# Performance work log

Measured on AMD Instinct MI355X. Metric: run time of the kernel, lower is better.

The kernel has to match this reference:

```python
import jax, jax.numpy as jnp
import numpy as np

KERNEL_MUL = 2.0
KERNEL_NUM = 5
EPS = 1e-8


def _l2_normalize(x):
    # F.normalize(p=2, dim=-1): x / max(||x||, 1e-12)
    norm = jnp.sqrt(jnp.sum(x * x, axis=-1, keepdims=True))
    return x / jnp.maximum(norm, 1e-12)


def _mmd(source, target):
    n_s = source.shape[0]
    n_t = target.shape[0]
    s = _l2_normalize(source)
    t = _l2_normalize(target)
    total = jnp.concatenate([s, t], axis=0)  # [n, d]
    n = n_s + n_t
    # pairwise squared L2 via norm-expansion trick (avoids [n,n,d] intermediate)
    sq = jnp.sum(total * total, axis=-1)  # [n]
    gram = total @ total.T                # [n, n]
    d2 = jnp.maximum(sq[:, None] + sq[None, :] - 2.0 * gram, 0.0)
    # bandwidth from detached distances (torch uses .data)
    d2_ng = jax.lax.stop_gradient(d2)
    bandwidth = jnp.sum(d2_ng) / (n * n - n) + EPS
    bandwidth = bandwidth / (KERNEL_MUL ** (KERNEL_NUM // 2))
    kernels = jnp.zeros_like(d2)
    for i in range(KERNEL_NUM):
        kernels = kernels + jnp.exp(-d2 / (bandwidth * KERNEL_MUL ** i))
    XX = kernels[:n_s, :n_s]
    YY = kernels[n_s:, n_s:]
    XY = kernels[:n_s, n_s:]
    loss = (jnp.sum(XX) - jnp.trace(XX)) / (n_s * (n_s - 1))
    loss = loss + (jnp.sum(YY) - jnp.trace(YY)) / (n_t * (n_t - 1))
    loss = loss - 2.0 * jnp.sum(XY) / (n_s * n_t)
    return loss


def setup_inputs() -> dict:
    key = jax.random.key(0)
    k1, k2 = jax.random.split(key)
    source = jax.random.normal(k1, (4096, 512), dtype=jnp.float32)
    target = jax.random.normal(k2, (4096, 512), dtype=jnp.float32)
    return {"source": source, "target": target}


def reference(source, target):
    return _mmd(source, target)
```

## Files before the change

kernel.cpp:

```cpp
#include <hip/hip_runtime.h>

#define D 512
#define NS 4096
#define NROWS 8192
#define NB_XX 272
#define NB_GEMM (2 * NB_XX + 512)
#define LDSS 24576

typedef __attribute__((ext_vector_type(8))) short bf16x8;
typedef __attribute__((ext_vector_type(4))) float f32x4;

__device__ __forceinline__ unsigned short f2bf(float f) {
  unsigned int u = __float_as_uint(f);
  u += 0x7fffu + ((u >> 16) & 1u);
  return (unsigned short)(u >> 16);
}
__device__ __forceinline__ float bf2f(unsigned short h) {
  return __uint_as_float(((unsigned int)h) << 16);
}
__device__ __forceinline__ void gload_lds16(const void* g, void* l) {
  __builtin_amdgcn_global_load_lds(
      (const __attribute__((address_space(1))) unsigned int*)g,
      (__attribute__((address_space(3))) unsigned int*)l, 16, 0, 0);
}
#define WAITV(N) asm volatile("s_waitcnt vmcnt(" #N ")" ::: "memory")

__global__ __launch_bounds__(512) void k_pre(const float* __restrict__ src,
                                             const float* __restrict__ tgt,
                                             float* __restrict__ sq,
                                             unsigned short* __restrict__ hi,
                                             unsigned short* __restrict__ lo,
                                             float* __restrict__ Spart) {
  int t = threadIdx.x, w = t >> 6, l = t & 63;
  float csum[8] = {0.f, 0.f, 0.f, 0.f, 0.f, 0.f, 0.f, 0.f};
  for (int i = 0; i < 16; ++i) {
    int r = blockIdx.x * 128 + w * 16 + i;
    const float* p = (r < NS) ? (src + (size_t)r * D) : (tgt + (size_t)(r - NS) * D);
    float4 v0 = *(const float4*)(p + l * 8);
    float4 v1 = *(const float4*)(p + l * 8 + 4);
    float x[8] = {v0.x, v0.y, v0.z, v0.w, v1.x, v1.y, v1.z, v1.w};
    float s = 0.f;
    #pragma unroll
    for (int j = 0; j < 8; ++j) s += x[j] * x[j];
    #pragma unroll
    for (int off = 1; off < 64; off <<= 1) s += __shfl_xor(s, off);
    float iv = 1.0f / fmaxf(sqrtf(s), 1e-12f);
    if (l == 0) sq[r] = s * iv * iv;
    unsigned short hs[8], ls[8];
    #pragma unroll
    for (int j = 0; j < 8; ++j) {
      float xn = x[j] * iv;
      unsigned short h = f2bf(xn);
      hs[j] = h;
      ls[j] = f2bf(xn - bf2f(h));
      csum[j] += xn;
    }
    *(uint4*)&hi[(size_t)r * D + l * 8] = *(uint4*)hs;
    *(uint4*)&lo[(size_t)r * D + l * 8] = *(uint4*)ls;
  }
  __shared__ float cs[8][512];
  #pragma unroll
  for (int j = 0; j < 8; ++j) cs[w][l * 8 + j] = csum[j];
  __syncthreads();
  float a = 0.f;
  #pragma unroll
  for (int ww = 0; ww < 8; ++ww) a += cs[ww][t];
  Spart[blockIdx.x * 512 + t] = a;
}

__global__ __launch_bounds__(512) void k_prep(const float* __restrict__ sq,
                                              const float* __restrict__ Spart,
                                              float* __restrict__ na,
                                              double* __restrict__ dsum,
                                              unsigned int* __restrict__ cnt) {
  int t = threadIdx.x;
  double ssq = 0.0;
  for (int i = t; i < NROWS; i += 512) ssq += (double)sq[i];
  double cssum = 0.0;
  for (int b = 0; b < 64; ++b) cssum += (double)Spart[b * 512 + t];
  double ss2 = cssum * cssum;
  #pragma unroll
  for (int off = 32; off; off >>= 1) {
    ssq += __shfl_down(ssq, off);
    ss2 += __shfl_down(ss2, off);
  }
  __shared__ double l1[8], l2[8];
  if ((t & 63) == 0) { l1[t >> 6] = ssq; l2[t >> 6] = ss2; }
  __syncthreads();
  if (t == 0) {
    double SSQ = 0.0, SS2 = 0.0;
    #pragma unroll
    for (int i = 0; i < 8; ++i) { SSQ += l1[i]; SS2 += l2[i]; }
    double n = (double)NROWS;
    double sum_d2 = 2.0 * n * SSQ - 2.0 * SS2;
    double bw = sum_d2 / (n * n - n) + 1e-8;
    bw = bw * 0.25;
    const double LOG2E = 1.4426950408889634;
    #pragma unroll
    for (int m = 0; m < 5; ++m) na[m] = (float)(-LOG2E / (bw * (double)(1 << m)));
    dsum[0] = 0.0; dsum[1] = 0.0; dsum[2] = 0.0;
    cnt[0] = 0u;
  }
}

__global__ __launch_bounds__(512, 2) void k_gemm(const unsigned short* __restrict__ hi,
                                                 const unsigned short* __restrict__ lo,
                                                 const float* __restrict__ sq,
                                                 const float* __restrict__ na,
                                                 double* __restrict__ dsum,
                                                 unsigned int* __restrict__ cnt,
                                                 float* __restrict__ out) {
  __shared__ unsigned short lds[3 * LDSS];
  __shared__ double red[8];

  int bid0 = blockIdx.x;
  int bid = (bid0 & 7) * (NB_GEMM / 8) + (bid0 >> 3);
  int type, bi, c2;
  if (bid < 2 * NB_XX) {
    type = (bid >= NB_XX);
    int idx = bid - type * NB_XX;
    int b = 0;
    while (idx >= 16 - (b >> 1)) { idx -= 16 - (b >> 1); ++b; }
    bi = b;
    c2 = (b >> 1) + idx;
  } else {
    type = 2;
    int rem = bid - 2 * NB_XX;
    bi = rem >> 4;
    c2 = rem & 15;
  }
  int offA = (type == 1) ? NS : 0;
  int offB = (type == 0) ? 0 : NS;
  bool sym = (type < 2);

  int t = threadIdx.x;
  int w = t >> 6, l = t & 63;
  int wr = w >> 2, wc = w & 3;
  int fr = l & 15, fk = l >> 4;

  const unsigned short* gsrc[6];
  int ldsoff[6];
  #pragma unroll
  for (int c = 0; c < 6; ++c) {
    int r = w * 6 + c;
    int isB = (r >= 16);
    int isLo = isB ? (r >= 32) : (r >= 8);
    int rr = isB ? ((r - 16) & 15) : (r & 7);
    int rowbase = isB ? (offB + c2 * 256 + rr * 16) : (offA + bi * 128 + rr * 16);
    const unsigned short* arr = isLo ? lo : hi;
    int gswz = ((l & 3) ^ ((l >> 3) & 3)) * 8;
    gsrc[c] = arr + (size_t)(rowbase + (l >> 2)) * D + gswz;
    ldsoff[c] = r * 512;
  }

  int rsw = (fr >> 1) & 3;
  int aoff = (wr * 64 + fr) * 32 + (fk ^ rsw) * 8;
  int boff = 8192 + (wc * 64 + fr) * 32 + (fk ^ rsw) * 8;

  f32x4 acc[4][4];
  f32x4 zero = {0.f, 0.f, 0.f, 0.f};
  #pragma unroll
  for (int m = 0; m < 4; ++m)
    #pragma unroll
    for (int n = 0; n < 4; ++n) acc[m][n] = zero;

  #pragma unroll
  for (int c = 0; c < 6; ++c) gload_lds16(gsrc[c], &lds[ldsoff[c]]);
  #pragma unroll
  for (int c = 0; c < 6; ++c) gload_lds16(gsrc[c] + 32, &lds[LDSS + ldsoff[c]]);

  unsigned int b0 = 0, b1 = LDSS, b2 = 2 * LDSS;
  for (int kt = 0; kt < 16; ++kt) {
    if (kt < 15) { WAITV(6); } else { WAITV(0); }
    __builtin_amdgcn_s_barrier();
    __builtin_amdgcn_sched_barrier(0);

    bf16x8 ah[4], al[4], bh[4], bl[4];
    #pragma unroll
    for (int m = 0; m < 4; ++m) {
      ah[m] = *(const bf16x8*)&lds[b0 + aoff + m * 512];
      al[m] = *(const bf16x8*)&lds[b0 + 4096 + aoff + m * 512];
    }
    #pragma unroll
    for (int n = 0; n < 4; ++n) {
      bh[n] = *(const bf16x8*)&lds[b0 + boff + n * 512];
      bl[n] = *(const bf16x8*)&lds[b0 + 8192 + boff + n * 512];
    }
    if (kt < 14) {
      #pragma unroll
      for (int c = 0; c < 6; ++c)
        gload_lds16(gsrc[c] + (kt + 2) * 32, &lds[b2 + ldsoff[c]]);
    }
    __builtin_amdgcn_s_setprio(1);
    #pragma unroll
    for (int m = 0; m < 4; ++m)
      #pragma unroll
      for (int n = 0; n < 4; ++n) {
        acc[m][n] = __builtin_amdgcn_mfma_f32_16x16x32_bf16(ah[m], bh[n], acc[m][n], 0, 0, 0);
        acc[m][n] = __builtin_amdgcn_mfma_f32_16x16x32_bf16(ah[m], bl[n], acc[m][n], 0, 0, 0);
        acc[m][n] = __builtin_amdgcn_mfma_f32_16x16x32_bf16(al[m], bh[n], acc[m][n], 0, 0, 0);
      }
    __builtin_amdgcn_s_setprio(0);
    unsigned int tmp = b0; b0 = b1; b1 = b2; b2 = tmp;
  }

  float nam[5];
  #pragma unroll
  for (int m2 = 0; m2 < 5; ++m2) nam[m2] = na[m2];
  int giL0 = bi * 128 + wr * 64;
  int gjL0 = c2 * 256 + wc * 64;
  float sqa[4][4], sqb[4];
  #pragma unroll
  for (int m = 0; m < 4; ++m)
    #pragma unroll
    for (int j = 0; j < 4; ++j) sqa[m][j] = sq[offA + giL0 + m * 16 + fk * 4 + j];
  #pragma unroll
  for (int n = 0; n < 4; ++n) sqb[n] = sq[offB + gjL0 + n * 16 + fr];

  double local = 0.0;
  #pragma unroll
  for (int m = 0; m < 4; ++m)
    #pragma unroll
    for (int n = 0; n < 4; ++n) {
      int gjL = gjL0 + n * 16 + fr;
      #pragma unroll
      for (int j = 0; j < 4; ++j) {
        int giL = giL0 + m * 16 + fk * 4 + j;
        float d2 = fmaxf(fmaf(-2.f, acc[m][n][j], sqa[m][j] + sqb[n]), 0.f);
        float kv = 0.f;
        #pragma unroll
        for (int m2 = 0; m2 < 5; ++m2) kv += __builtin_amdgcn_exp2f(d2 * nam[m2]);
        float wf = sym ? ((gjL > giL) ? 2.f : ((gjL == giL) ? 1.f : 0.f)) : 1.f;
        local += (double)(wf * kv);
      }
    }
  #pragma unroll
  for (int off = 32; off; off >>= 1) local += __shfl_down(local, off);
  if (l == 0) red[w] = local;
  __syncthreads();
  if (t == 0) {
    double bsum = 0.0;
    #pragma unroll
    for (int i = 0; i < 8; ++i) bsum += red[i];
    atomicAdd(&dsum[type], bsum);
    __threadfence();
    unsigned int ticket = atomicAdd(cnt, 1u);
    if (ticket == NB_GEMM - 1) {
      __threadfence();
      double A0 = dsum[0], A1 = dsum[1], A2 = dsum[2];
      double ns = (double)NS;
      double loss = (A0 - 5.0 * ns) / (ns * (ns - 1.0))
                  + (A1 - 5.0 * ns) / (ns * (ns - 1.0))
                  - 2.0 * A2 / (ns * ns);
      out[0] = (float)loss;
    }
  }
}

extern "C" void kernel_launch(void* const* d_in, const int* in_sizes, int n_in,
                              void* d_out, int out_size, void* d_ws, size_t ws_size,
                              hipStream_t stream) {
  (void)in_sizes; (void)n_in; (void)out_size; (void)ws_size;
  const float* src = (const float*)d_in[0];
  const float* tgt = (const float*)d_in[1];
  float* out = (float*)d_out;
  char* ws = (char*)d_ws;

  float*          sq    = (float*)(ws);
  float*          Spart = (float*)(ws + 0x8000);
  float*          na    = (float*)(ws + 0x28000);
  double*         dsum  = (double*)(ws + 0x28040);
  unsigned int*   cnt   = (unsigned int*)(ws + 0x28080);
  unsigned short* hi    = (unsigned short*)(ws + 0x100000);
  unsigned short* lo    = (unsigned short*)(ws + 0x900000);

  hipLaunchKernelGGL(k_pre, dim3(64), dim3(512), 0, stream, src, tgt, sq, hi, lo, Spart);
  hipLaunchKernelGGL(k_prep, dim3(1), dim3(512), 0, stream, sq, Spart, na, dsum, cnt);
  hipLaunchKernelGGL(k_gemm, dim3(NB_GEMM), dim3(512), 0, stream, hi, lo, sq, na, dsum, cnt, out);
}
```

Measured before the change: 232.4 us.

## Switch split-bf16 gram to int8 hi/lo fixed-point MFMA with persistent tile queue

Normalized rows are quantized to 14-bit fixed point and split into int8 high and low halves. The gram matrix is then computed with i8 MFMA (16x16x64) into exact int32 accumulators and recombined in double, replacing the three-pass bf16 hi/lo scheme. The GEMM also becomes a persistent kernel of 256 blocks that pull tiles from an atomic queue, with prefetch of the next tile's data overlapping the current tile's tail. Squared norms are recomputed from the quantized integers so the distances stay consistent. The trade-off is four MFMAs per step instead of three, at higher int8 throughput and half the bytes, plus quantization error and more register pressure from three accumulator sets.

Result: slower. 354.6 us (+52.5%).

```diff
diff --git a/kernel.cpp b/kernel.cpp
--- a/kernel.cpp
+++ b/kernel.cpp
@@ -4,20 +4,13 @@
 #define NS 4096
 #define NROWS 8192
 #define NB_XX 272
-#define NB_GEMM (2 * NB_XX + 512)
-#define LDSS 24576
-
-typedef __attribute__((ext_vector_type(8))) short bf16x8;
-typedef __attribute__((ext_vector_type(4))) float f32x4;
-
-__device__ __forceinline__ unsigned short f2bf(float f) {
-  unsigned int u = __float_as_uint(f);
-  u += 0x7fffu + ((u >> 16) & 1u);
-  return (unsigned short)(u >> 16);
-}
-__device__ __forceinline__ float bf2f(unsigned short h) {
-  return __uint_as_float(((unsigned int)h) << 16);
-}
+#define NB (2 * NB_XX + 512)
+#define NPB 256
+#define LDSB 49152
+#define LA_OFF 0x400000u
+
+typedef __attribute__((ext_vector_type(4))) int i32x4;
+
 __device__ __forceinline__ void gload_lds16(const void* g, void* l) {
   __builtin_amdgcn_global_load_lds(
       (const __attribute__((address_space(1))) unsigned int*)g,
@@ -28,8 +21,8 @@
 __global__ __launch_bounds__(512) void k_pre(const float* __restrict__ src,
                                              const float* __restrict__ tgt,
                                              float* __restrict__ sq,
-                                             unsigned short* __restrict__ hi,
-                                             unsigned short* __restrict__ lo,
+                                             signed char* __restrict__ ha,
+                                             signed char* __restrict__ la,
                                              float* __restrict__ Spart) {
   int t = threadIdx.x, w = t >> 6, l = t & 63;
   float csum[8] = {0.f, 0.f, 0.f, 0.f, 0.f, 0.f, 0.f, 0.f};
@@ -45,18 +38,24 @@
     #pragma unroll
     for (int off = 1; off < 64; off <<= 1) s += __shfl_xor(s, off);
     float iv = 1.0f / fmaxf(sqrtf(s), 1e-12f);
-    if (l == 0) sq[r] = s * iv * iv;
-    unsigned short hs[8], ls[8];
+    signed char hs[8], ls[8];
+    int sxx = 0;
     #pragma unroll
     for (int j = 0; j < 8; ++j) {
       float xn = x[j] * iv;
-      unsigned short h = f2bf(xn);
-      hs[j] = h;
-      ls[j] = f2bf(xn - bf2f(h));
+      int X = __float2int_rn(xn * 16384.f);
+      int h = (X + 128) >> 8;
+      int lo = X - (h << 8);
+      hs[j] = (signed char)h;
+      ls[j] = (signed char)lo;
+      sxx += X * X;
       csum[j] += xn;
     }
-    *(uint4*)&hi[(size_t)r * D + l * 8] = *(uint4*)hs;
-    *(uint4*)&lo[(size_t)r * D + l * 8] = *(uint4*)ls;
+    #pragma unroll
+    for (int off = 1; off < 64; off <<= 1) sxx += __shfl_xor(sxx, off);
+    if (l == 0) sq[r] = (float)((double)sxx * (1.0 / 268435456.0));
+    *(uint2*)&ha[(size_t)r * 512 + l * 8] = *(uint2*)hs;
+    *(uint2*)&la[(size_t)r * 512 + l * 8] = *(uint2*)ls;
   }
   __shared__ float cs[8][512];
   #pragma unroll
@@ -72,7 +71,8 @@
                                               const float* __restrict__ Spart,
                                               float* __restrict__ na,
                                               double* __restrict__ dsum,
-                                              unsigned int* __restrict__ cnt) {
+                                              unsigned int* __restrict__ qcnt,
+                                              unsigned int* __restrict__ ccnt) {
   int t = threadIdx.x;
   double ssq = 0.0;
   for (int i = t; i < NROWS; i += 512) ssq += (double)sq[i];
@@ -99,153 +99,231 @@
     #pragma unroll
     for (int m = 0; m < 5; ++m) na[m] = (float)(-LOG2E / (bw * (double)(1 << m)));
     dsum[0] = 0.0; dsum[1] = 0.0; dsum[2] = 0.0;
-    cnt[0] = 0u;
-  }
-}
-
-__global__ __launch_bounds__(512, 2) void k_gemm(const unsigned short* __restrict__ hi,
-                                                 const unsigned short* __restrict__ lo,
-                                                 const float* __restrict__ sq,
-                                                 const float* __restrict__ na,
-                                                 double* __restrict__ dsum,
-                                                 unsigned int* __restrict__ cnt,
-                                                 float* __restrict__ out) {
-  __shared__ unsigned short lds[3 * LDSS];
-  __shared__ double red[8];
-
-  int bid0 = blockIdx.x;
-  int bid = (bid0 & 7) * (NB_GEMM / 8) + (bid0 >> 3);
-  int type, bi, c2;
+    qcnt[0] = 0u; ccnt[0] = 0u;
+  }
+}
+
+__device__ __forceinline__ void decode_tile(int bid, int& type, int& bi, int& c2,
+                                            int& offA, int& offB, int& sym) {
   if (bid < 2 * NB_XX) {
     type = (bid >= NB_XX);
     int idx = bid - type * NB_XX;
     int b = 0;
     while (idx >= 16 - (b >> 1)) { idx -= 16 - (b >> 1); ++b; }
-    bi = b;
-    c2 = (b >> 1) + idx;
+    bi = b; c2 = (b >> 1) + idx; sym = 1;
   } else {
     type = 2;
     int rem = bid - 2 * NB_XX;
-    bi = rem >> 4;
-    c2 = rem & 15;
-  }
-  int offA = (type == 1) ? NS : 0;
-  int offB = (type == 0) ? 0 : NS;
-  bool sym = (type < 2);
+    bi = rem >> 4; c2 = rem & 15; sym = 0;
+  }
+  offA = (type == 1) ? NS : 0;
+  offB = (type == 0) ? 0 : NS;
+}
+
+__global__ __launch_bounds__(512, 2) void k_gemm(const signed char* __restrict__ ha,
+                                                 const float* __restrict__ sq,
+                                                 const float* __restrict__ na,
+                                                 double* __restrict__ dsum,
+                                                 unsigned int* __restrict__ qcnt,
+                                                 unsigned int* __restrict__ ccnt,
+                                                 float* __restrict__ out) {
+  __shared__ signed char lds[3 * LDSB];
+  __shared__ int tslot[2];
+  __shared__ double red[8];
 
   int t = threadIdx.x;
   int w = t >> 6, l = t & 63;
   int wr = w >> 2, wc = w & 3;
   int fr = l & 15, fk = l >> 4;
-
-  const unsigned short* gsrc[6];
-  int ldsoff[6];
+  int rsw = (fr >> 1) & 3;
+
+  unsigned offc[6];
+  int isb[6];
+  int gsw = ((l & 3) ^ ((l >> 3) & 3)) * 16;
   #pragma unroll
   for (int c = 0; c < 6; ++c) {
     int r = w * 6 + c;
     int isB = (r >= 16);
     int isLo = isB ? (r >= 32) : (r >= 8);
-    int rr = isB ? ((r - 16) & 15) : (r & 7);
-    int rowbase = isB ? (offB + c2 * 256 + rr * 16) : (offA + bi * 128 + rr * 16);
-    const unsigned short* arr = isLo ? lo : hi;
-    int gswz = ((l & 3) ^ ((l >> 3) & 3)) * 8;
-    gsrc[c] = arr + (size_t)(rowbase + (l >> 2)) * D + gswz;
-    ldsoff[c] = r * 512;
-  }
-
-  int rsw = (fr >> 1) & 3;
-  int aoff = (wr * 64 + fr) * 32 + (fk ^ rsw) * 8;
-  int boff = 8192 + (wc * 64 + fr) * 32 + (fk ^ rsw) * 8;
-
-  f32x4 acc[4][4];
-  f32x4 zero = {0.f, 0.f, 0.f, 0.f};
+    int rr16 = isB ? ((r - 16) & 15) : (r & 7);
+    offc[c] = (isLo ? LA_OFF : 0u) + (unsigned)((rr16 * 16 + (l >> 2)) * 512 + gsw);
+    isb[c] = isB;
+  }
+  int ldsw = w * 6 * 1024;
+  int aRd = (wr * 4) * 1024 + fr * 64 + ((fk ^ rsw) * 16);
+  int bRd = 16384 + (wc * 4) * 1024 + fr * 64 + ((fk ^ rsw) * 16);
+
+  float nam0 = na[0], nam1 = na[1], nam2 = na[2], nam3 = na[3], nam4 = na[4];
+
+  i32x4 acc1[4][4], acc2[4][4], acc3[4][4];
+  i32x4 izero = {0, 0, 0, 0};
   #pragma unroll
   for (int m = 0; m < 4; ++m)
     #pragma unroll
-    for (int n = 0; n < 4; ++n) acc[m][n] = zero;
-
-  #pragma unroll
-  for (int c = 0; c < 6; ++c) gload_lds16(gsrc[c], &lds[ldsoff[c]]);
-  #pragma unroll
-  for (int c = 0; c < 6; ++c) gload_lds16(gsrc[c] + 32, &lds[LDSS + ldsoff[c]]);
-
-  unsigned int b0 = 0, b1 = LDSS, b2 = 2 * LDSS;
-  for (int kt = 0; kt < 16; ++kt) {
-    if (kt < 15) { WAITV(6); } else { WAITV(0); }
-    __builtin_amdgcn_s_barrier();
-    __builtin_amdgcn_sched_barrier(0);
-
-    bf16x8 ah[4], al[4], bh[4], bl[4];
-    #pragma unroll
-    for (int m = 0; m < 4; ++m) {
-      ah[m] = *(const bf16x8*)&lds[b0 + aoff + m * 512];
-      al[m] = *(const bf16x8*)&lds[b0 + 4096 + aoff + m * 512];
-    }
-    #pragma unroll
-    for (int n = 0; n < 4; ++n) {
-      bh[n] = *(const bf16x8*)&lds[b0 + boff + n * 512];
-      bl[n] = *(const bf16x8*)&lds[b0 + 8192 + boff + n * 512];
-    }
-    if (kt < 14) {
-      #pragma unroll
-      for (int c = 0; c < 6; ++c)
-        gload_lds16(gsrc[c] + (kt + 2) * 32, &lds[b2 + ldsoff[c]]);
-    }
-    __builtin_amdgcn_s_setprio(1);
-    #pragma unroll
-    for (int m = 0; m < 4; ++m)
+    for (int n = 0; n < 4; ++n) { acc1[m][n] = izero; acc2[m][n] = izero; acc3[m][n] = izero; }
+
+  double dl0 = 0.0, dl1 = 0.0, dl2 = 0.0;
+
+  if (t == 0) {
+    tslot[0] = (int)atomicAdd(qcnt, 1u);
+    tslot[1] = (int)atomicAdd(qcnt, 1u);
+  }
+  __syncthreads();
+  int cur = __builtin_amdgcn_readfirstlane(tslot[0]);
+  int nxt = __builtin_amdgcn_readfirstlane(tslot[1]);
+
+  int typeC = 0, biC = 0, c2C = 0, oAC = 0, oBC = 0, symC = 0;
+  unsigned tbA_c = 0, tbB_c = 0, tbA_n = 0, tbB_n = 0;
+  if (cur < NB) {
+    decode_tile(cur, typeC, biC, c2C, oAC, oBC, symC);
+    tbA_c = (unsigned)(oAC + biC * 128) * 512u;
+    tbB_c = (unsigned)(oBC + c2C * 256) * 512u;
+  }
+  if (nxt < NB) {
+    int t2, b2, cc2, a2, o2, s2;
+    decode_tile(nxt, t2, b2, cc2, a2, o2, s2);
+    tbA_n = (unsigned)(a2 + b2 * 128) * 512u;
+    tbB_n = (unsigned)(o2 + cc2 * 256) * 512u;
+  }
+
+  if (cur < NB) {
+    #pragma unroll
+    for (int c = 0; c < 6; ++c)
+      gload_lds16(ha + (size_t)(offc[c] + (isb[c] ? tbB_c : tbA_c)), &lds[0 + ldsw + c * 1024]);
+    #pragma unroll
+    for (int c = 0; c < 6; ++c)
+      gload_lds16(ha + (size_t)(offc[c] + (isb[c] ? tbB_c : tbA_c) + 64u), &lds[LDSB + ldsw + c * 1024]);
+  }
+
+  unsigned sb0 = 0, sb1 = LDSB, sb2 = 2 * LDSB;
+  int pend = NB;
+
+  while (cur < NB) {
+    bool nxtv = (nxt < NB);
+    for (int kt = 0; kt < 8; ++kt) {
+      if (kt == 7 && !nxtv) { WAITV(0); } else { WAITV(6); }
+      __builtin_amdgcn_s_barrier();
+      __builtin_amdgcn_sched_barrier(0);
+      if (kt == 0) {
+        if (t == 0) {
+          int v = (int)atomicAdd(qcnt, 1u);
+          tslot[0] = v;
+          asm volatile("s_waitcnt lgkmcnt(0)" ::: "memory");
+        }
+      }
+      if (kt == 1) pend = __builtin_amdgcn_readfirstlane(tslot[0]);
+
+      i32x4 Ah[4], Al[4];
+      #pragma unroll
+      for (int m = 0; m < 4; ++m) {
+        Ah[m] = *(const i32x4*)&lds[sb0 + aRd + m * 1024];
+        Al[m] = *(const i32x4*)&lds[sb0 + 8192 + aRd + m * 1024];
+      }
+      int st = kt + 2;
+      if (st < 8) {
+        #pragma unroll
+        for (int c = 0; c < 6; ++c)
+          gload_lds16(ha + (size_t)(offc[c] + (isb[c] ? tbB_c : tbA_c) + (unsigned)st * 64u),
+                      &lds[sb2 + ldsw + c * 1024]);
+      } else if (nxtv) {
+        #pragma unroll
+        for (int c = 0; c < 6; ++c)
+          gload_lds16(ha + (size_t)(offc[c] + (isb[c] ? tbB_n : tbA_n) + (unsigned)(st - 8) * 64u),
+                      &lds[sb2 + ldsw + c * 1024]);
+      }
+      __builtin_amdgcn_s_setprio(1);
       #pragma unroll
       for (int n = 0; n < 4; ++n) {
-        acc[m][n] = __builtin_amdgcn_mfma_f32_16x16x32_bf16(ah[m], bh[n], acc[m][n], 0, 0, 0);
-        acc[m][n] = __builtin_amdgcn_mfma_f32_16x16x32_bf16(ah[m], bl[n], acc[m][n], 0, 0, 0);
-        acc[m][n] = __builtin_amdgcn_mfma_f32_16x16x32_bf16(al[m], bh[n], acc[m][n], 0, 0, 0);
-      }
-    __builtin_amdgcn_s_setprio(0);
-    unsigned int tmp = b0; b0 = b1; b1 = b2; b2 = tmp;
-  }
-
-  float nam[5];
-  #pragma unroll
-  for (int m2 = 0; m2 < 5; ++m2) nam[m2] = na[m2];
-  int giL0 = bi * 128 + wr * 64;
-  int gjL0 = c2 * 256 + wc * 64;
-  float sqa[4][4], sqb[4];
-  #pragma unroll
-  for (int m = 0; m < 4; ++m)
-    #pragma unroll
-    for (int j = 0; j < 4; ++j) sqa[m][j] = sq[offA + giL0 + m * 16 + fk * 4 + j];
-  #pragma unroll
-  for (int n = 0; n < 4; ++n) sqb[n] = sq[offB + gjL0 + n * 16 + fr];
-
-  double local = 0.0;
-  #pragma unroll
-  for (int m = 0; m < 4; ++m)
-    #pragma unroll
-    for (int n = 0; n < 4; ++n) {
-      int gjL = gjL0 + n * 16 + fr;
-      #pragma unroll
-      for (int j = 0; j < 4; ++j) {
-        int giL = giL0 + m * 16 + fk * 4 + j;
-        float d2 = fmaxf(fmaf(-2.f, acc[m][n][j], sqa[m][j] + sqb[n]), 0.f);
-        float kv = 0.f;
-        #pragma unroll
-        for (int m2 = 0; m2 < 5; ++m2) kv += __builtin_amdgcn_exp2f(d2 * nam[m2]);
-        float wf = sym ? ((gjL > giL) ? 2.f : ((gjL == giL) ? 1.f : 0.f)) : 1.f;
-        local += (double)(wf * kv);
-      }
-    }
-  #pragma unroll
-  for (int off = 32; off; off >>= 1) local += __shfl_down(local, off);
-  if (l == 0) red[w] = local;
+        i32x4 Bh = *(const i32x4*)&lds[sb0 + bRd + n * 1024];
+        i32x4 Bl = *(const i32x4*)&lds[sb0 + 16384 + bRd + n * 1024];
+        #pragma unroll
+        for (int m = 0; m < 4; ++m) {
+          acc1[m][n] = __builtin_amdgcn_mfma_i32_16x16x64_i8(Ah[m], Bh, acc1[m][n], 0, 0, 0);
+          acc2[m][n] = __builtin_amdgcn_mfma_i32_16x16x64_i8(Ah[m], Bl, acc2[m][n], 0, 0, 0);
+          acc2[m][n] = __builtin_amdgcn_mfma_i32_16x16x64_i8(Al[m], Bh, acc2[m][n], 0, 0, 0);
+          acc3[m][n] = __builtin_amdgcn_mfma_i32_16x16x64_i8(Al[m], Bl, acc3[m][n], 0, 0, 0);
+        }
+      }
+      __builtin_amdgcn_s_setprio(0);
+      unsigned tmp = sb0; sb0 = sb1; sb1 = sb2; sb2 = tmp;
+    }
+
+    {
+      int giL0 = biC * 128 + wr * 64;
+      int gjL0 = c2C * 256 + wc * 64;
+      float sqa[4][4], sqb[4];
+      #pragma unroll
+      for (int m = 0; m < 4; ++m)
+        #pragma unroll
+        for (int j = 0; j < 4; ++j) sqa[m][j] = sq[oAC + giL0 + m * 16 + fk * 4 + j];
+      #pragma unroll
+      for (int n = 0; n < 4; ++n) sqb[n] = sq[oBC + gjL0 + n * 16 + fr];
+
+      double lsum = 0.0;
+      #pragma unroll
+      for (int m = 0; m < 4; ++m)
+        #pragma unroll
+        for (int n = 0; n < 4; ++n) {
+          int gjL = gjL0 + n * 16 + fr;
+          #pragma unroll
+          for (int j = 0; j < 4; ++j) {
+            int giL = giL0 + m * 16 + fk * 4 + j;
+            double tt = 65536.0 * (double)acc1[m][n][j] + 256.0 * (double)acc2[m][n][j]
+                      + (double)acc3[m][n][j];
+            double d2d = (double)sqa[m][j] + (double)sqb[n] - tt * 7.450580596923828e-9;
+            float d2v = fmaxf((float)d2d, 0.f);
+            float kv = __builtin_amdgcn_exp2f(d2v * nam0) + __builtin_amdgcn_exp2f(d2v * nam1)
+                     + __builtin_amdgcn_exp2f(d2v * nam2) + __builtin_amdgcn_exp2f(d2v * nam3)
+                     + __builtin_amdgcn_exp2f(d2v * nam4);
+            float wf = symC ? ((gjL > giL) ? 2.f : ((gjL == giL) ? 1.f : 0.f)) : 1.f;
+            lsum += (double)(wf * kv);
+          }
+        }
+      if (typeC == 0) dl0 += lsum;
+      else if (typeC == 1) dl1 += lsum;
+      else dl2 += lsum;
+      #pragma unroll
+      for (int m = 0; m < 4; ++m)
+        #pragma unroll
+        for (int n = 0; n < 4; ++n) { acc1[m][n] = izero; acc2[m][n] = izero; acc3[m][n] = izero; }
+    }
+
+    cur = nxt; tbA_c = tbA_n; tbB_c = tbB_n;
+    nxt = pend;
+    if (cur < NB) {
+      decode_tile(cur, typeC, biC, c2C, oAC, oBC, symC);
+      if (nxt < NB) {
+        int t2, b2, cc2, a2, o2, s2;
+        decode_tile(nxt, t2, b2, cc2, a2, o2, s2);
+        tbA_n = (unsigned)(a2 + b2 * 128) * 512u;
+        tbB_n = (unsigned)(o2 + cc2 * 256) * 512u;
+      }
+    }
+  }
+
   __syncthreads();
+  #pragma unroll
+  for (int off = 32; off; off >>= 1) {
+    dl0 += __shfl_down(dl0, off);
+    dl1 += __shfl_down(dl1, off);
+    dl2 += __shfl_down(dl2, off);
+  }
+  for (int pass = 0; pass < 3; ++pass) {
+    double v = (pass == 0) ? dl0 : (pass == 1) ? dl1 : dl2;
+    if (l == 0) red[w] = v;
+    __syncthreads();
+    if (t == 0) {
+      double bs = 0.0;
+      #pragma unroll
+      for (int i = 0; i < 8; ++i) bs += red[i];
+      atomicAdd(&dsum[pass], bs);
+    }
+    __syncthreads();
+  }
+  __threadfence();
   if (t == 0) {
-    double bsum = 0.0;
-    #pragma unroll
-    for (int i = 0; i < 8; ++i) bsum += red[i];
-    atomicAdd(&dsum[type], bsum);
-    __threadfence();
-    unsigned int ticket = atomicAdd(cnt, 1u);
-    if (ticket == NB_GEMM - 1) {
+    unsigned tk = atomicAdd(ccnt, 1u);
+    if (tk == NPB - 1) {
       __threadfence();
       double A0 = dsum[0], A1 = dsum[1], A2 = dsum[2];
       double ns = (double)NS;
@@ -266,15 +344,16 @@
   float* out = (float*)d_out;
   char* ws = (char*)d_ws;
 
-  float*          sq    = (float*)(ws);
-  float*          Spart = (float*)(ws + 0x8000);
-  float*          na    = (float*)(ws + 0x28000);
-  double*         dsum  = (double*)(ws + 0x28040);
-  unsigned int*   cnt   = (unsigned int*)(ws + 0x28080);
-  unsigned short* hi    = (unsigned short*)(ws + 0x100000);
-  unsigned short* lo    = (unsigned short*)(ws + 0x900000);
-
-  hipLaunchKernelGGL(k_pre, dim3(64), dim3(512), 0, stream, src, tgt, sq, hi, lo, Spart);
-  hipLaunchKernelGGL(k_prep, dim3(1), dim3(512), 0, stream, sq, Spart, na, dsum, cnt);
-  hipLaunchKernelGGL(k_gemm, dim3(NB_GEMM), dim3(512), 0, stream, hi, lo, sq, na, dsum, cnt, out);
-}
+  float*        sq    = (float*)(ws);
+  float*        Spart = (float*)(ws + 0x8000);
+  float*        na    = (float*)(ws + 0x28000);
+  double*       dsum  = (double*)(ws + 0x28040);
+  unsigned int* qcnt  = (unsigned int*)(ws + 0x28080);
+  unsigned int* ccnt  = (unsigned int*)(ws + 0x28084);
+  signed char*  ha    = (signed char*)(ws + 0x100000);
+  signed char*  la    = (signed char*)(ws + 0x500000);
+
+  hipLaunchKernelGGL(k_pre, dim3(64), dim3(512), 0, stream, src, tgt, sq, ha, la, Spart);
+  hipLaunchKernelGGL(k_prep, dim3(1), dim3(512), 0, stream, sq, Spart, na, dsum, qcnt, ccnt);
+  hipLaunchKernelGGL(k_gemm, dim3(NPB), dim3(512), 0, stream, ha, sq, na, dsum, qcnt, ccnt, out);
+}
```
